# Optimization experiments

Measured on AMD Instinct MI355X. Metric: run time of the kernel, lower is better.

Reference implementation:

```python
import jax, jax.numpy as jnp
import numpy as np

B, S, D_IN, D_OUT = 4, 2048, 1024, 1024


def setup_inputs() -> dict:
    key = jax.random.key(0)
    k1, k2, k3, k4 = jax.random.split(key, 4)
    x = jax.random.normal(k1, (B, S, D_IN), dtype=jnp.float32)
    scale = 1.0 / np.sqrt(D_IN)
    Wq = jax.random.normal(k2, (D_IN, D_OUT), dtype=jnp.float32) * scale
    Wk = jax.random.normal(k3, (D_IN, D_OUT), dtype=jnp.float32) * scale
    Wv = jax.random.normal(k4, (D_IN, D_OUT), dtype=jnp.float32) * scale
    return {"x": x, "Wq": Wq, "Wk": Wk, "Wv": Wv}


def reference(x, Wq, Wk, Wv):
    # QKV projections (Linear, no bias)
    q = jnp.einsum('bsd,de->bse', x, Wq)  # [B,S,D_OUT]
    k = jnp.einsum('bsd,de->bse', x, Wk)
    v = jnp.einsum('bsd,de->bse', x, Wv)
    d_out = Wq.shape[1]
    # raw scores [B,S,S], scaled after masking (identical math: -inf stays -inf)
    scores = jnp.einsum('bqe,bke->bqk', q, k) * (d_out ** -0.5)
    S_ = x.shape[1]
    # causal mask: future positions (j > i) are masked out
    causal = jnp.triu(jnp.ones((S_, S_), dtype=bool), k=1)
    scores = jnp.where(causal[None, :, :], -jnp.inf, scores)
    attn = jax.nn.softmax(scores, axis=-1)  # dropout p=0.0 -> identity
    return jnp.einsum('bqk,bke->bqe', attn, v)
```

## Files before the change

### kernel.cpp

```cpp
#include <hip/hip_runtime.h>
#include <stdint.h>

typedef unsigned short u16;
typedef unsigned int u32;
typedef __bf16 bf16x8 __attribute__((ext_vector_type(8)));
typedef float f32x4 __attribute__((ext_vector_type(4)));
typedef float f32x16 __attribute__((ext_vector_type(16)));

#define BM 128
#define BN 128
#define BK 64

__device__ __forceinline__ u16 f2bf(float x) {
  union { float f; uint32_t u; } c; c.f = x;
  uint32_t r = (c.u + 0x7FFFu + ((c.u >> 16) & 1u)) >> 16;
  return (u16)r;
}

__device__ __forceinline__ void async_copy16(const u16* g, u16* l) {
  __builtin_amdgcn_global_load_lds(
      (const __attribute__((address_space(1))) void*)g,
      (__attribute__((address_space(3))) void*)l,
      16, 0, 0);
}

__global__ void zerofill_u16(u16* __restrict__ p) {
  long i = (long)blockIdx.x * 256 + threadIdx.x;
  p[i] = 0;
}

__global__ __launch_bounds__(256)
void prep(const void* __restrict__ xs, const void* __restrict__ w0,
          const void* __restrict__ w1, const void* __restrict__ w2,
          u16* __restrict__ xn, u16* __restrict__ WT3, u32* __restrict__ flag,
          int nxb)
{
  __shared__ int sh_hits;
  __shared__ u16 tile[64][72];
  if (threadIdx.x == 0) sh_hits = 0;
  __syncthreads();
  {
    const u16* w = (const u16*)w0;
    int h = 0;
    for (int i = threadIdx.x; i < 8192; i += 256)
      if ((w[i] & 0x7F80u) == 0x7F80u) h++;
    if (h) atomicAdd(&sh_hits, h);
  }
  __syncthreads();
  const bool isf32 = (sh_hits > 0);
  const int blk = blockIdx.x;
  const int tid = threadIdx.x;
  if (blk == 0 && tid == 0) *flag = isf32 ? 1000u : 0u;

  if (blk < nxb) {
    long i = ((long)blk * 256 + tid) * 8;
    u16 o[8];
    if (isf32) {
      const float* s = (const float*)xs + i;
      f32x4 a = *(const f32x4*)s;
      f32x4 b = *(const f32x4*)(s + 4);
#pragma unroll
      for (int c = 0; c < 4; ++c) { o[c] = f2bf(a[c]); o[c + 4] = f2bf(b[c]); }
    } else {
      *(uint4*)o = *(const uint4*)((const u16*)xs + i);
    }
    *(uint4*)(xn + i) = *(uint4*)o;
  } else {
    const int Dd = 1024;
    int t = blk - nxb;
    int z = t >> 8;
    int r = t & 255;
    const int r0 = (r >> 4) * 64, c0 = (r & 15) * 64;
    const void* src = (z == 0) ? w0 : (z == 1) ? w1 : w2;
    u16* out = WT3 + (long)z * Dd * Dd;
#pragma unroll
    for (int p = 0; p < 2; ++p) {
      int v = tid + p * 256;
      int row = v >> 3, c8 = (v & 7) * 8;
      u16 tt[8];
      if (isf32) {
        const float* sp = (const float*)src + (long)(r0 + row) * Dd + c0 + c8;
        f32x4 a = *(const f32x4*)sp;
        f32x4 b = *(const f32x4*)(sp + 4);
#pragma unroll
        for (int c = 0; c < 4; ++c) { tt[c] = f2bf(a[c]); tt[c + 4] = f2bf(b[c]); }
      } else {
        *(uint4*)tt = *(const uint4*)((const u16*)src + (long)(r0 + row) * Dd + c0 + c8);
      }
#pragma unroll
      for (int c = 0; c < 8; ++c) tile[row][c8 + c] = tt[c];
    }
    __syncthreads();
#pragma unroll
    for (int p = 0; p < 2; ++p) {
      int v = tid + p * 256;
      int oc = v >> 3, r8 = (v & 7) * 8;
      union { uint4 q; u16 s[8]; } tt;
#pragma unroll
      for (int c = 0; c < 8; ++c) tt.s[c] = tile[r8 + c][oc];
      *(uint4*)(out + (long)(c0 + oc) * Dd + r0 + r8) = tt.q;
    }
  }
}

template <int MODE>
__global__ __launch_bounds__(256, 2)
void gemm_nt(const u16* __restrict__ A, const u16* __restrict__ B, void* __restrict__ Cv,
             const u32* __restrict__ flag,
             int K, int lda, int ldb, int ldc,
             long sA, long sB, long sC, long cOff,
             float scale, int causal, int trik)
{
  int bm = blockIdx.y;
  if (trik) bm = gridDim.y - 1 - bm;
  const int bn = blockIdx.x, bz = blockIdx.z;
  if (causal && bn > bm) return;

  __shared__ u16 As[BM * BK];
  __shared__ u16 Bs[BN * BK];

  A += (long)bz * sA;
  B += (long)bz * sB;

  const int tid  = threadIdx.x;
  const int wid  = tid >> 6;
  const int lane = tid & 63;
  const int l32  = lane & 31;
  const int lh   = lane >> 5;
  const int srow = lane >> 3;
  const int swz  = ((lane & 7) ^ srow) * 8;
  const int m0 = bm * BM, n0 = bn * BN;

  int nk = K / BK;
  if (trik) { int lim = (m0 + BM) / BK; if (lim < nk) nk = lim; }

  f32x16 acc[2][2] = {};

  for (int kt = 0; kt < nk; ++kt) {
    const int k0 = kt * BK;
#pragma unroll
    for (int c = 0; c < 4; ++c) {
      const int rb = wid * 32 + c * 8;
      async_copy16(A + (long)(m0 + rb + srow) * lda + (k0 + swz), As + rb * BK);
      async_copy16(B + (long)(n0 + rb + srow) * ldb + (k0 + swz), Bs + rb * BK);
    }
    __syncthreads();
#pragma unroll
    for (int ks = 0; ks < 4; ++ks) {
      bf16x8 av[2], bv[2];
      const int cb = ((ks * 2 + lh) ^ (lane & 7)) * 8;
#pragma unroll
      for (int i = 0; i < 2; ++i) {
        const int Ra = (wid >> 1) * 64 + i * 32 + l32;
        const int Rb = (wid & 1)  * 64 + i * 32 + l32;
        av[i] = *(const bf16x8*)(As + Ra * BK + cb);
        bv[i] = *(const bf16x8*)(Bs + Rb * BK + cb);
      }
#pragma unroll
      for (int mi = 0; mi < 2; ++mi)
#pragma unroll
        for (int ni = 0; ni < 2; ++ni)
          acc[mi][ni] = __builtin_amdgcn_mfma_f32_32x32x16_bf16(av[mi], bv[ni], acc[mi][ni], 0, 0, 0);
    }
    __syncthreads();
  }

  const int rb0 = m0 + (wid >> 1) * 64;
  const int cb0 = n0 + (wid & 1) * 64;
  const long cbase = (long)bz * sC + cOff;
  const bool f32out = (MODE == 1) || (MODE == 2 && *flag > 32);

#pragma unroll
  for (int mi = 0; mi < 2; ++mi)
#pragma unroll
    for (int ni = 0; ni < 2; ++ni) {
      const int col = cb0 + ni * 32 + l32;
#pragma unroll
      for (int reg = 0; reg < 16; ++reg) {
        const int row = rb0 + mi * 32 + (reg & 3) + 8 * (reg >> 2) + 4 * lh;
        const float v = acc[mi][ni][reg] * scale;
        const long idx = cbase + (long)row * ldc + col;
        if constexpr (MODE == 0) {
          ((u16*)Cv)[idx] = f2bf(v);
        } else if constexpr (MODE == 1) {
          ((float*)Cv)[idx] = v;
        } else {
          if (f32out) ((float*)Cv)[idx] = v;
          else        ((u16*)Cv)[idx]   = f2bf(v);
        }
      }
    }
}

__global__ __launch_bounds__(256)
void transpose_bf16(const u16* __restrict__ in, u16* __restrict__ out,
                    int ldIn, int ldOut, long sIn, long sOut)
{
  __shared__ u16 tile[64][72];
  const int bz = blockIdx.z;
  in  += (long)bz * sIn;
  out += (long)bz * sOut;
  const int r0 = blockIdx.y * 64, c0 = blockIdx.x * 64;
  const int tid = threadIdx.x;
#pragma unroll
  for (int p = 0; p < 2; ++p) {
    int v = tid + p * 256;
    int row = v >> 3, c8 = (v & 7) * 8;
    union { uint4 q; u16 s[8]; } t;
    t.q = *(const uint4*)(in + (long)(r0 + row) * ldIn + c0 + c8);
#pragma unroll
    for (int i = 0; i < 8; ++i) tile[row][c8 + i] = t.s[i];
  }
  __syncthreads();
#pragma unroll
  for (int p = 0; p < 2; ++p) {
    int v = tid + p * 256;
    int oc = v >> 3, r8 = (v & 7) * 8;
    union { uint4 q; u16 s[8]; } t;
#pragma unroll
    for (int i = 0; i < 8; ++i) t.s[i] = tile[r8 + i][oc];
    *(uint4*)(out + (long)(c0 + oc) * ldOut + r0 + r8) = t.q;
  }
}

__global__ __launch_bounds__(256)
void softmax_causal(char* __restrict__ base, long rowStrideB, int modS)
{
  const long r = blockIdx.x;
  const int i = (int)(r % modS);
  float* sc = (float*)(base + r * rowStrideB);
  u16*   pr = (u16*)(base + r * rowStrideB);
  const int n = i + 1;
  const int tid = threadIdx.x;
  const int j0 = tid * 8;
  const int wv = tid >> 6, lane = tid & 63;
  __shared__ float red[4];

  float e[8];
  float m = -3.0e38f;
  if (j0 < n) {
    f32x4 a = *(const f32x4*)(sc + j0);
    f32x4 b = *(const f32x4*)(sc + j0 + 4);
#pragma unroll
    for (int c = 0; c < 4; ++c) { e[c] = a[c]; e[c + 4] = b[c]; }
#pragma unroll
    for (int c = 0; c < 8; ++c) {
      if (j0 + c < n) m = fmaxf(m, e[c]); else e[c] = -3.0e38f;
    }
  } else {
#pragma unroll
    for (int c = 0; c < 8; ++c) e[c] = -3.0e38f;
  }
#pragma unroll
  for (int o = 32; o > 0; o >>= 1) m = fmaxf(m, __shfl_xor(m, o));
  if (lane == 0) red[wv] = m;
  __syncthreads();
  m = fmaxf(fmaxf(red[0], red[1]), fmaxf(red[2], red[3]));
  __syncthreads();

  float s = 0.f;
#pragma unroll
  for (int c = 0; c < 8; ++c) { float x = __expf(e[c] - m); e[c] = x; s += x; }
#pragma unroll
  for (int o = 32; o > 0; o >>= 1) s += __shfl_xor(s, o);
  if (lane == 0) red[wv] = s;
  __syncthreads();
  s = red[0] + red[1] + red[2] + red[3];
  const float inv = 1.0f / s;

  u16 o8[8];
#pragma unroll
  for (int c = 0; c < 8; ++c) o8[c] = f2bf(e[c] * inv);
  *(uint4*)(pr + j0) = *(uint4*)o8;
}

extern "C" void kernel_launch(void* const* d_in, const int* in_sizes, int n_in,
                              void* d_out, int out_size, void* d_ws, size_t ws_size,
                              hipStream_t stream)
{
  (void)in_sizes; (void)n_in; (void)out_size;
  const int Bb = 4, S = 2048, D = 1024, D3 = 3072;
  const long SD = (long)S * D;
  const long SS = (long)S * S;
  const long N_X = (long)Bb * SD;
  const long N_W = (long)D * D;

  char* ws = (char*)d_ws;
  size_t off = 0;
  auto take = [&](size_t bytes) -> void* {
    void* p = ws + off;
    off = (off + bytes + 255) & ~((size_t)255);
    return p;
  };

  u32* flag = (u32*)take(4096);
  u16* xn   = (u16*)take((size_t)N_X * 2);
  u16* WT3  = (u16*)take((size_t)3 * N_W * 2);
  const size_t off_common = off;

  const size_t needA = off_common + (size_t)(N_X * 3 * 2)
                     + (size_t)(N_X * 2)
                     + (size_t)(Bb * SS * 4) + 4096;
  const size_t needC = off_common + (size_t)(S * (long)D3 * 2)
                     + (size_t)(SD * 2)
                     + (size_t)(SS * 4) + 4096;

  if (ws_size < needC) {
    zerofill_u16<<<(int)(N_X / 256), 256, 0, stream>>>((u16*)d_out);
    return;
  }

  const int nxb = (int)(N_X / 2048);
  prep<<<nxb + 768, 256, 0, stream>>>(d_in[0], d_in[1], d_in[2], d_in[3],
                                      xn, WT3, flag, nxb);

  const float scl = 0.03125f;

  if (ws_size >= needA) {
    u16*   QKV = (u16*)take((size_t)N_X * 3 * 2);
    u16*   VT  = (u16*)take((size_t)N_X * 2);
    float* sc  = (float*)take((size_t)Bb * SS * 4);

    gemm_nt<0><<<dim3(D3 / BN, (int)(N_X / D) / BM, 1), 256, 0, stream>>>(
        xn, WT3, QKV, flag, D, D, D, D3, 0, 0, 0, 0, 1.f, 0, 0);

    transpose_bf16<<<dim3(D / 64, S / 64, Bb), 256, 0, stream>>>(
        QKV + 2048, VT, D3, S, (long)S * D3, SD);

    gemm_nt<1><<<dim3(S / BN, S / BM, Bb), 256, 0, stream>>>(
        QKV, QKV + 1024, sc, flag, D, D3, D3, S,
        (long)S * D3, (long)S * D3, SS, 0, scl, 1, 0);

    softmax_causal<<<Bb * S, 256, 0, stream>>>((char*)sc, (long)S * 4, S);

    gemm_nt<2><<<dim3(D / BN, S / BM, Bb), 256, 0, stream>>>(
        (u16*)sc, VT, d_out, flag, S, 2 * S, S, D,
        2 * SS, SD, SD, 0, 1.f, 0, 1);
  } else {
    u16*   QKVb = (u16*)take((size_t)S * D3 * 2);
    u16*   VTb  = (u16*)take((size_t)SD * 2);
    float* scb  = (float*)take((size_t)SS * 4);

    for (int b = 0; b < Bb; ++b) {
      gemm_nt<0><<<dim3(D3 / BN, S / BM, 1), 256, 0, stream>>>(
          xn + (long)b * SD, WT3, QKVb, flag, D, D, D, D3, 0, 0, 0, 0, 1.f, 0, 0);

      transpose_bf16<<<dim3(D / 64, S / 64, 1), 256, 0, stream>>>(
          QKVb + 2048, VTb, D3, S, 0, 0);

      gemm_nt<1><<<dim3(S / BN, S / BM, 1), 256, 0, stream>>>(
          QKVb, QKVb + 1024, scb, flag, D, D3, D3, S, 0, 0, 0, 0, scl, 1, 0);

      softmax_causal<<<S, 256, 0, stream>>>((char*)scb, (long)S * 4, S);

      gemm_nt<2><<<dim3(D / BN, S / BM, 1), 256, 0, stream>>>(
          (u16*)scb, VTb, d_out, flag, S, 2 * S, S, D,
          0, 0, 0, (long)b * SD, 1.f, 0, 1);
    }
  }
}
```

Before: 267.7 us.

## Switch GEMM to 16x16x32 MFMA and launch only lower-triangular score tiles

The shared GEMM kernel now uses 16x16x32 bf16 MFMA instructions with a 4x4 accumulator grid per wave instead of 32x32x16 with a 2x2 grid, which changes LDS fragment loads and the epilogue store pattern. The causal score GEMM is launched over a compact 1D triangular grid and maps block indices to (bm, bn) with a sqrt-based decode. This removes the roughly half of launched blocks that previously exited early. The smaller MFMA shape may give different throughput and a narrower store footprint per lane.

```diff
diff --git a/kernel.cpp b/kernel.cpp
--- a/kernel.cpp
+++ b/kernel.cpp
@@ -5,7 +5,6 @@
 typedef unsigned int u32;
 typedef __bf16 bf16x8 __attribute__((ext_vector_type(8)));
 typedef float f32x4 __attribute__((ext_vector_type(4)));
-typedef float f32x16 __attribute__((ext_vector_type(16)));
 
 #define BM 128
 #define BN 128
@@ -111,10 +110,20 @@
              long sA, long sB, long sC, long cOff,
              float scale, int causal, int trik)
 {
-  int bm = blockIdx.y;
-  if (trik) bm = gridDim.y - 1 - bm;
-  const int bn = blockIdx.x, bz = blockIdx.z;
-  if (causal && bn > bm) return;
+  int bm, bn;
+  if (causal == 2) {
+    int t = blockIdx.x;
+    bm = (int)((__fsqrt_rn(8.0f * (float)t + 1.0f) - 1.0f) * 0.5f);
+    while ((bm + 1) * (bm + 2) / 2 <= t) ++bm;
+    while (bm * (bm + 1) / 2 > t) --bm;
+    bn = t - bm * (bm + 1) / 2;
+  } else {
+    bm = blockIdx.y;
+    if (trik) bm = gridDim.y - 1 - bm;
+    bn = blockIdx.x;
+    if (causal == 1 && bn > bm) return;
+  }
+  const int bz = blockIdx.z;
 
   __shared__ u16 As[BM * BK];
   __shared__ u16 Bs[BN * BK];
@@ -125,8 +134,8 @@
   const int tid  = threadIdx.x;
   const int wid  = tid >> 6;
   const int lane = tid & 63;
-  const int l32  = lane & 31;
-  const int lh   = lane >> 5;
+  const int l16  = lane & 15;
+  const int lk   = lane >> 4;
   const int srow = lane >> 3;
   const int swz  = ((lane & 7) ^ srow) * 8;
   const int m0 = bm * BM, n0 = bn * BN;
@@ -134,7 +143,7 @@
   int nk = K / BK;
   if (trik) { int lim = (m0 + BM) / BK; if (lim < nk) nk = lim; }
 
-  f32x16 acc[2][2] = {};
+  f32x4 acc[4][4] = {};
 
   for (int kt = 0; kt < nk; ++kt) {
     const int k0 = kt * BK;
@@ -146,21 +155,21 @@
     }
     __syncthreads();
 #pragma unroll
-    for (int ks = 0; ks < 4; ++ks) {
-      bf16x8 av[2], bv[2];
-      const int cb = ((ks * 2 + lh) ^ (lane & 7)) * 8;
-#pragma unroll
-      for (int i = 0; i < 2; ++i) {
-        const int Ra = (wid >> 1) * 64 + i * 32 + l32;
-        const int Rb = (wid & 1)  * 64 + i * 32 + l32;
-        av[i] = *(const bf16x8*)(As + Ra * BK + cb);
-        bv[i] = *(const bf16x8*)(Bs + Rb * BK + cb);
+    for (int kh = 0; kh < 2; ++kh) {
+      bf16x8 av[4], bv[4];
+#pragma unroll
+      for (int i = 0; i < 4; ++i) {
+        const int Ra = (wid >> 1) * 64 + i * 16 + l16;
+        const int Rb = (wid & 1)  * 64 + i * 16 + l16;
+        const int ca = ((kh * 4 + lk) ^ (l16 & 7)) * 8;
+        av[i] = *(const bf16x8*)(As + Ra * BK + ca);
+        bv[i] = *(const bf16x8*)(Bs + Rb * BK + ca);
       }
 #pragma unroll
-      for (int mi = 0; mi < 2; ++mi)
-#pragma unroll
-        for (int ni = 0; ni < 2; ++ni)
-          acc[mi][ni] = __builtin_amdgcn_mfma_f32_32x32x16_bf16(av[mi], bv[ni], acc[mi][ni], 0, 0, 0);
+      for (int mi = 0; mi < 4; ++mi)
+#pragma unroll
+        for (int ni = 0; ni < 4; ++ni)
+          acc[mi][ni] = __builtin_amdgcn_mfma_f32_16x16x32_bf16(av[mi], bv[ni], acc[mi][ni], 0, 0, 0);
     }
     __syncthreads();
   }
@@ -171,15 +180,15 @@
   const bool f32out = (MODE == 1) || (MODE == 2 && *flag > 32);
 
 #pragma unroll
-  for (int mi = 0; mi < 2; ++mi)
-#pragma unroll
-    for (int ni = 0; ni < 2; ++ni) {
-      const int col = cb0 + ni * 32 + l32;
-#pragma unroll
-      for (int reg = 0; reg < 16; ++reg) {
-        const int row = rb0 + mi * 32 + (reg & 3) + 8 * (reg >> 2) + 4 * lh;
-        const float v = acc[mi][ni][reg] * scale;
-        const long idx = cbase + (long)row * ldc + col;
+  for (int mi = 0; mi < 4; ++mi)
+#pragma unroll
+    for (int ni = 0; ni < 4; ++ni) {
+      const int row = rb0 + mi * 16 + lk * 4;
+      const int col = cb0 + ni * 16 + l16;
+#pragma unroll
+      for (int r = 0; r < 4; ++r) {
+        const float v = acc[mi][ni][r] * scale;
+        const long idx = cbase + (long)(row + r) * ldc + col;
         if constexpr (MODE == 0) {
           ((u16*)Cv)[idx] = f2bf(v);
         } else if constexpr (MODE == 1) {
@@ -284,6 +293,7 @@
   const long SS = (long)S * S;
   const long N_X = (long)Bb * SD;
   const long N_W = (long)D * D;
+  const int NTRI = 16 * 17 / 2;
 
   char* ws = (char*)d_ws;
   size_t off = 0;
@@ -327,9 +337,9 @@
     transpose_bf16<<<dim3(D / 64, S / 64, Bb), 256, 0, stream>>>(
         QKV + 2048, VT, D3, S, (long)S * D3, SD);
 
-    gemm_nt<1><<<dim3(S / BN, S / BM, Bb), 256, 0, stream>>>(
+    gemm_nt<1><<<dim3(NTRI, 1, Bb), 256, 0, stream>>>(
         QKV, QKV + 1024, sc, flag, D, D3, D3, S,
-        (long)S * D3, (long)S * D3, SS, 0, scl, 1, 0);
+        (long)S * D3, (long)S * D3, SS, 0, scl, 2, 0);
 
     softmax_causal<<<Bb * S, 256, 0, stream>>>((char*)sc, (long)S * 4, S);
 
@@ -348,8 +358,8 @@
       transpose_bf16<<<dim3(D / 64, S / 64, 1), 256, 0, stream>>>(
           QKVb + 2048, VTb, D3, S, 0, 0);
 
-      gemm_nt<1><<<dim3(S / BN, S / BM, 1), 256, 0, stream>>>(
-          QKVb, QKVb + 1024, scb, flag, D, D3, D3, S, 0, 0, 0, 0, scl, 1, 0);
+      gemm_nt<1><<<dim3(NTRI, 1, 1), 256, 0, stream>>>(
+          QKVb, QKVb + 1024, scb, flag, D, D3, D3, S, 0, 0, 0, 0, scl, 2, 0);
 
       softmax_causal<<<S, 256, 0, stream>>>((char*)scb, (long)S * 4, S);
 
```

Measured after the change: 264.1 us. Within noise of the previous version (-1.3%).
